# Optimization experiments

Measured on AMD Instinct MI355X. Metric: run time of the kernel, lower is better.

Reference implementation:

```python
import jax, jax.numpy as jnp
import numpy as np

# Criterion init constants
WEIGHT_START = 1e-3
WEIGHT_MAX = 5e3
START_RAMPUP = 50000
N_RAMPUP = 100000
EPS = 1e-3

B, N_CLOTH, M_OBS, N_FACES = 2, 16384, 12000, 16384


def setup_inputs() -> dict:
    key = jax.random.key(0)
    ks = jax.random.split(key, 5)
    return dict(
        cloth_curr_pos=jax.random.normal(ks[0], (B, N_CLOTH, 3), jnp.float32),
        cloth_next_pos=jax.random.normal(ks[1], (B, N_CLOTH, 3), jnp.float32),
        obstacle_curr_pos=jax.random.normal(ks[2], (B, M_OBS, 3), jnp.float32),
        obstacle_next_pos=jax.random.normal(ks[3], (B, M_OBS, 3), jnp.float32),
        obstacle_faces=jax.random.randint(ks[4], (B, N_FACES, 3), 0, M_OBS, dtype=jnp.int64),
        iter_num=60000,
    )


def _face_normals(verts, faces):
    # verts: [M,3], faces: [F,3] -> normalized face normals [F,3]
    v = verts[faces]  # [F,3(vert),3(xyz)]
    n = jnp.cross(v[:, 1] - v[:, 0], v[:, 2] - v[:, 0])
    return n / (jnp.linalg.norm(n, axis=-1, keepdims=True) + 1e-12)


def _calc_loss(curr_pos, next_pos, obs_curr, obs_next, faces):
    # face centroids at current obstacle positions: [F,3]
    face_curr = obs_curr[faces].mean(axis=-2)
    # brute-force KNN (K=1): squared euclidean distances [N,F]
    d2 = (
        jnp.sum(curr_pos * curr_pos, axis=-1, keepdims=True)
        - 2.0 * curr_pos @ face_curr.T
        + jnp.sum(face_curr * face_curr, axis=-1)[None, :]
    )
    nn_idx = jnp.argmin(d2, axis=-1)  # [N]
    # face centroids / normals at next obstacle positions
    face_next = obs_next[faces].mean(axis=-2)  # [F,3]
    fn = _face_normals(obs_next, faces)        # [F,3]
    nn_points = face_next[nn_idx]   # [N,3]
    nn_normals = fn[nn_idx]         # [N,3]
    distance = jnp.sum((next_pos - nn_points) * nn_normals, axis=-1)  # [N]
    interpenetration = jnp.maximum(EPS - distance, 0.0) ** 3
    return interpenetration.sum(), interpenetration


def reference(cloth_curr_pos, cloth_next_pos, obstacle_curr_pos, obstacle_next_pos, obstacle_faces, iter_num):
    # weight ramp (Python scalar math, matches get_weight)
    it = max(iter_num - START_RAMPUP, 0)
    progress = min(it / N_RAMPUP, 1.0)
    weight = WEIGHT_START + (WEIGHT_MAX - WEIGHT_START) * progress

    losses, per_verts = jax.vmap(_calc_loss)(
        cloth_curr_pos, cloth_next_pos, obstacle_curr_pos, obstacle_next_pos, obstacle_faces
    )
    b = cloth_curr_pos.shape[0]
    loss = losses.sum() / b * weight          # scalar
    per_vert = per_verts.sum(axis=0) / b * weight  # [N]
    return loss, per_vert
```

## Files before the change

kernel.cpp:

```cpp
#include <hip/hip_runtime.h>
#include <math.h>

#define B_ 2
#define N_ 16384
#define M_ 12000
#define F_ 16384

#define P_ 128
#define TILE_ 128
#define NCHUNK_ 8

typedef short bf16x8 __attribute__((ext_vector_type(8)));
typedef float f32x16 __attribute__((ext_vector_type(16)));

__device__ __host__ inline unsigned short bf16rn(float x) {
  unsigned int u = __float_as_uint(x);
  u = (u + 0x7FFFu + ((u >> 16) & 1u)) >> 16;
  return (unsigned short)u;
}
__device__ inline float bf16tof(unsigned short h) {
  return __uint_as_float(((unsigned int)h) << 16);
}

__device__ __forceinline__ void gload_lds16(const uint4* g, uint4* l) {
  __builtin_amdgcn_global_load_lds(
      (const __attribute__((address_space(1))) void*)g,
      (__attribute__((address_space(3))) void*)l, 16, 0, 0);
}

__global__ __launch_bounds__(128) void face_precomp(
    const float* __restrict__ obs_curr,
    const float* __restrict__ obs_next,
    const int* __restrict__ faces,
    float4* __restrict__ fcurr,
    float4* __restrict__ fnext,
    uint4* __restrict__ fpack,
    float* __restrict__ out) {
  int lane = threadIdx.x & 63;
  int half = threadIdx.x >> 6;
  int t = blockIdx.x * 64 + lane;
  if (blockIdx.x == 0 && threadIdx.x == 0) out[0] = 0.0f;
  int b = t / F_;
  const int* fidx3 = faces + 3 * (size_t)t;
  int i0 = fidx3[0];
  int i1 = fidx3[1];
  int i2 = fidx3[2];

  if (half == 0) {
    const float* oc = obs_curr + (size_t)b * M_ * 3;
    float ax = oc[3*i0], ay = oc[3*i0+1], az = oc[3*i0+2];
    float bx = oc[3*i1], by = oc[3*i1+1], bz = oc[3*i1+2];
    float cx = oc[3*i2], cy = oc[3*i2+1], cz = oc[3*i2+2];
    float gx = (ax + bx + cx) / 3.0f;
    float gy = (ay + by + cy) / 3.0f;
    float gz = (az + bz + cz) / 3.0f;
    float w = gx*gx + gy*gy + gz*gz;
    fcurr[t] = make_float4(gx, gy, gz, w);

    float fx = -2.0f * gx, fy = -2.0f * gy, fz = -2.0f * gz;
    unsigned short fhx = bf16rn(fx), flx = bf16rn(fx - bf16tof(fhx));
    unsigned short fhy = bf16rn(fy), fly = bf16rn(fy - bf16tof(fhy));
    unsigned short fhz = bf16rn(fz), flz = bf16rn(fz - bf16tof(fhz));
    unsigned short whi = bf16rn(w),  wlo = bf16rn(w - bf16tof(whi));
    uint4 r0, r1;
    r0.x = (unsigned)fhx | ((unsigned)flx << 16);
    r0.y = r0.x;
    r0.z = (unsigned)fhy | ((unsigned)fly << 16);
    r0.w = r0.z;
    r1.x = (unsigned)fhz | ((unsigned)flz << 16);
    r1.y = r1.x;
    r1.z = (unsigned)whi | ((unsigned)wlo << 16);
    r1.w = 0;
    fpack[(size_t)t * 2 + 0] = r0;
    fpack[(size_t)t * 2 + 1] = r1;
  } else {
    const float* on = obs_next + (size_t)b * M_ * 3;
    float nax = on[3*i0], nay = on[3*i0+1], naz = on[3*i0+2];
    float nbx = on[3*i1], nby = on[3*i1+1], nbz = on[3*i1+2];
    float ncx = on[3*i2], ncy = on[3*i2+1], ncz = on[3*i2+2];
    float hx = (nax + nbx + ncx) / 3.0f;
    float hy = (nay + nby + ncy) / 3.0f;
    float hz = (naz + nbz + ncz) / 3.0f;
    float e1x = nbx - nax, e1y = nby - nay, e1z = nbz - naz;
    float e2x = ncx - nax, e2y = ncy - nay, e2z = ncz - naz;
    float crx = e1y * e2z - e1z * e2y;
    float cry = e1z * e2x - e1x * e2z;
    float crz = e1x * e2y - e1y * e2x;
    float len = sqrtf(crx*crx + cry*cry + crz*crz);
    float inv = 1.0f / (len + 1e-12f);
    fnext[2 * (size_t)t + 0] = make_float4(hx, hy, hz, 0.0f);
    fnext[2 * (size_t)t + 1] = make_float4(crx*inv, cry*inv, crz*inv, 0.0f);
  }
}

__global__ __launch_bounds__(256, 4) void knn_mfma32(
    const float* __restrict__ cloth_curr,
    const uint4* __restrict__ fpack,
    float2* __restrict__ pchunk) {
  __shared__ uint4 abuf[2][256];

  int bid = blockIdx.x;
  int s   = bid & 7;
  int vb  = (bid >> 3) & 63;
  int b   = bid >> 9;
  int lane = threadIdx.x & 63;
  int wid  = threadIdx.x >> 6;
  int h = lane >> 5;
  int m = lane & 31;
  int vw = vb * 256 + wid * 64;

  const short one = (short)0x3F80;
  bf16x8 bfrag0, bfrag1;
#pragma unroll
  for (int g = 0; g < 2; ++g) {
    const float* cp = cloth_curr + ((size_t)b * N_ + vw + g * 32 + m) * 3;
    float cxx = cp[0], cyy = cp[1], czz = cp[2];
    unsigned short chx = bf16rn(cxx), clx = bf16rn(cxx - bf16tof(chx));
    unsigned short chy = bf16rn(cyy), cly = bf16rn(cyy - bf16tof(chy));
    unsigned short chz = bf16rn(czz), clz = bf16rn(czz - bf16tof(chz));
    bf16x8 tq;
    if (h == 0) {
      tq[0] = (short)chx; tq[1] = (short)chx;
      tq[2] = (short)clx; tq[3] = (short)clx;
      tq[4] = (short)chy; tq[5] = (short)chy;
      tq[6] = (short)cly; tq[7] = (short)cly;
    } else {
      tq[0] = (short)chz; tq[1] = (short)chz;
      tq[2] = (short)clz; tq[3] = (short)clz;
      tq[4] = one; tq[5] = one;
      tq[6] = 0;   tq[7] = 0;
    }
    if (g == 0) bfrag0 = tq; else bfrag1 = tq;
  }

  f32x16 zc;
#pragma unroll
  for (int k = 0; k < 16; ++k) zc[k] = 0.0f;

  const uint4* chunk = fpack + ((size_t)b * F_ + (size_t)s * 2048) * 2;

  gload_lds16(chunk + wid * 64 + lane, &abuf[0][wid * 64]);
  __syncthreads();

  float rb0 = 3.4e38f, rb1 = 3.4e38f;
  int   rp0 = 0,       rp1 = 0;

  for (int part = 0; part < 16; ++part) {
    int cur = part & 1;
    if (part < 15)
      gload_lds16(chunk + (part + 1) * 256 + wid * 64 + lane,
                  &abuf[cur ^ 1][wid * 64]);

    float r0[8], r1[8];
#pragma unroll
    for (int k = 0; k < 8; ++k) { r0[k] = 3.4e38f; r1[k] = 3.4e38f; }

    const uint4* lp = &abuf[cur][m * 2 + h];
#pragma unroll
    for (int grp = 0; grp < 2; ++grp) {
      uint4 a0 = lp[grp * 128];
      uint4 a1 = lp[grp * 128 + 64];
      bf16x8 av0 = __builtin_bit_cast(bf16x8, a0);
      bf16x8 av1 = __builtin_bit_cast(bf16x8, a1);
      f32x16 d00 = __builtin_amdgcn_mfma_f32_32x32x16_bf16(av0, bfrag0, zc, 0, 0, 0);
      f32x16 d01 = __builtin_amdgcn_mfma_f32_32x32x16_bf16(av0, bfrag1, zc, 0, 0, 0);
      f32x16 d10 = __builtin_amdgcn_mfma_f32_32x32x16_bf16(av1, bfrag0, zc, 0, 0, 0);
      f32x16 d11 = __builtin_amdgcn_mfma_f32_32x32x16_bf16(av1, bfrag1, zc, 0, 0, 0);
#pragma unroll
      for (int k = 0; k < 8; ++k) {
        r0[k] = fminf(fminf(d00[k], d00[k + 8]), r0[k]);
        r0[k] = fminf(fminf(d10[k], d10[k + 8]), r0[k]);
        r1[k] = fminf(fminf(d01[k], d01[k + 8]), r1[k]);
        r1[k] = fminf(fminf(d11[k], d11[k + 8]), r1[k]);
      }
    }
    float t0 = fminf(fminf(r0[0], r0[1]), r0[2]);
    t0 = fminf(fminf(t0, r0[3]), r0[4]);
    t0 = fminf(fminf(t0, r0[5]), r0[6]);
    float bmin0 = fminf(t0, r0[7]);
    float t1 = fminf(fminf(r1[0], r1[1]), r1[2]);
    t1 = fminf(fminf(t1, r1[3]), r1[4]);
    t1 = fminf(fminf(t1, r1[5]), r1[6]);
    float bmin1 = fminf(t1, r1[7]);
    bmin0 = fminf(bmin0, __shfl_xor(bmin0, 32, 64));
    bmin1 = fminf(bmin1, __shfl_xor(bmin1, 32, 64));

    bool u0 = bmin0 < rb0;
    rb0 = u0 ? bmin0 : rb0;
    rp0 = u0 ? part : rp0;
    bool u1 = bmin1 < rb1;
    rb1 = u1 ? bmin1 : rb1;
    rp1 = u1 ? part : rp1;

    if (part < 15) __syncthreads();
  }

  float2* pout = pchunk + ((size_t)(b * NCHUNK_ + s)) * N_ + vw;
  if (lane < 32) {
    pout[lane]      = make_float2(rb0, __int_as_float(s * 16 + rp0));
    pout[32 + lane] = make_float2(rb1, __int_as_float(s * 16 + rp1));
  }
}

__global__ __launch_bounds__(128) void epilogue(
    const float* __restrict__ cloth_curr,
    const float* __restrict__ cloth_next,
    const float4* __restrict__ fcurr,
    const float4* __restrict__ fnext,
    const float2* __restrict__ pchunk,
    const int* __restrict__ iter_num,
    float* __restrict__ out) {
  int t = blockIdx.x * 128 + threadIdx.x;
  int i = t >> 1;
  int b = t & 1;

  int it = *iter_num;
  double itc = (double)(it - 50000);
  if (itc < 0.0) itc = 0.0;
  double prog = itc / 100000.0;
  if (prog > 1.0) prog = 1.0;
  float weight = (float)(1e-3 + (5e3 - 1e-3) * prog);
  float scale = weight * 0.5f;

  const float* cp = cloth_curr + ((size_t)b * N_ + i) * 3;
  float m2x = -2.0f * cp[0];
  float m2y = -2.0f * cp[1];
  float m2z = -2.0f * cp[2];
  const float* np2 = cloth_next + ((size_t)b * N_ + i) * 3;
  float nx = np2[0], ny = np2[1], nz = np2[2];

  float best = 3.4e38f;
  int bp = 0;
#pragma unroll
  for (int c = 0; c < NCHUNK_; ++c) {
    float2 v = pchunk[((size_t)(b * NCHUNK_ + c)) * N_ + i];
    bool mm = v.x < best;
    best = mm ? v.x : best;
    bp = mm ? __float_as_int(v.y) : bp;
  }

  const float4* fpp = fcurr + (size_t)b * F_ + (size_t)bp * TILE_;
  float sbest = 3.4e38f;
  int jwin = 0;
#pragma unroll 8
  for (int j = 0; j < TILE_; ++j) {
    float4 fc = fpp[j];
    float s = fmaf(m2x, fc.x, fmaf(m2y, fc.y, fmaf(m2z, fc.z, fc.w)));
    bool u = s < sbest;
    sbest = u ? s : sbest;
    jwin = u ? j : jwin;
  }
  int fidx = bp * TILE_ + jwin;

  float4 cent = fnext[2 * ((size_t)b * F_ + fidx) + 0];
  float4 nrm  = fnext[2 * ((size_t)b * F_ + fidx) + 1];
  float dist = (nx - cent.x) * nrm.x +
               (ny - cent.y) * nrm.y +
               (nz - cent.z) * nrm.z;
  float ip = fmaxf(1e-3f - dist, 0.0f);
  float acc = ip * ip * ip * scale;

  float pair = acc + __shfl_xor(acc, 1, 64);
  if (b == 0) out[1 + i] = pair;

  float r = acc;
#pragma unroll
  for (int off = 32; off > 0; off >>= 1) r += __shfl_down(r, off, 64);
  __shared__ float wsum[2];
  int lane = threadIdx.x & 63;
  int w = threadIdx.x >> 6;
  if (lane == 0) wsum[w] = r;
  __syncthreads();
  if (threadIdx.x == 0)
    atomicAdd(out, wsum[0] + wsum[1]);
}

extern "C" void kernel_launch(void* const* d_in, const int* in_sizes, int n_in,
                              void* d_out, int out_size, void* d_ws, size_t ws_size,
                              hipStream_t stream) {
  const float* cloth_curr = (const float*)d_in[0];
  const float* cloth_next = (const float*)d_in[1];
  const float* obs_curr   = (const float*)d_in[2];
  const float* obs_next   = (const float*)d_in[3];
  const int*   faces      = (const int*)d_in[4];
  const int*   iter_num   = (const int*)d_in[5];
  float* out = (float*)d_out;

  char* w = (char*)d_ws;
  float4* fcurr = (float4*)(w);
  float4* fnext = (float4*)(w + 524288);
  uint4*  fpack = (uint4*)(w + 1572864);
  float2* pchunk = (float2*)(w + 3670016);

  face_precomp<<<(B_ * F_) / 64, 128, 0, stream>>>(
      obs_curr, obs_next, faces, fcurr, fnext, fpack, out);

  knn_mfma32<<<1024, 256, 0, stream>>>(cloth_curr, fpack, pchunk);

  epilogue<<<(2 * N_ + 127) / 128, 128, 0, stream>>>(
      cloth_curr, cloth_next, fcurr, fnext, pchunk, iter_num, out);
}
```

Before: 104.5 us.

## Fuse epilogue into KNN kernel via last-block-done atomic counter

Removes the separate epilogue launch. Each KNN block bumps a per-vertex-block counter, and the last of the 16 blocks (8 chunks times 2 batches) for a 256-vertex group does the chunk reduction, the tile rescan, the interpenetration and the sum. The counter is reset inside face_precomp. This saves one kernel launch and its gap, at the cost of threadfences, atomics and a serial tail done by the last-arriving blocks.

```diff
diff --git a/kernel.cpp b/kernel.cpp
--- a/kernel.cpp
+++ b/kernel.cpp
@@ -35,11 +35,13 @@
     float4* __restrict__ fcurr,
     float4* __restrict__ fnext,
     uint4* __restrict__ fpack,
-    float* __restrict__ out) {
+    float* __restrict__ out,
+    int* __restrict__ cnt) {
   int lane = threadIdx.x & 63;
   int half = threadIdx.x >> 6;
   int t = blockIdx.x * 64 + lane;
   if (blockIdx.x == 0 && threadIdx.x == 0) out[0] = 0.0f;
+  if (blockIdx.x == 0 && half == 1) cnt[lane] = 0;
   int b = t / F_;
   const int* fidx3 = faces + 3 * (size_t)t;
   int i0 = fidx3[0];
@@ -96,7 +98,13 @@
 __global__ __launch_bounds__(256, 4) void knn_mfma32(
     const float* __restrict__ cloth_curr,
     const uint4* __restrict__ fpack,
-    float2* __restrict__ pchunk) {
+    float2* __restrict__ pchunk,
+    const float* __restrict__ cloth_next,
+    const float4* __restrict__ fcurr,
+    const float4* __restrict__ fnext,
+    const int* __restrict__ iter_num,
+    float* __restrict__ out,
+    int* __restrict__ cnt) {
   __shared__ uint4 abuf[2][256];
 
   int bid = blockIdx.x;
@@ -200,79 +208,95 @@
     pout[lane]      = make_float2(rb0, __int_as_float(s * 16 + rp0));
     pout[32 + lane] = make_float2(rb1, __int_as_float(s * 16 + rp1));
   }
-}
-
-__global__ __launch_bounds__(128) void epilogue(
-    const float* __restrict__ cloth_curr,
-    const float* __restrict__ cloth_next,
-    const float4* __restrict__ fcurr,
-    const float4* __restrict__ fnext,
-    const float2* __restrict__ pchunk,
-    const int* __restrict__ iter_num,
-    float* __restrict__ out) {
-  int t = blockIdx.x * 128 + threadIdx.x;
-  int i = t >> 1;
-  int b = t & 1;
-
-  int it = *iter_num;
-  double itc = (double)(it - 50000);
+
+  __syncthreads();
+  __shared__ int lastflag;
+  if (threadIdx.x == 0) {
+    __threadfence();
+    int old = atomicAdd(&cnt[vb], 1);
+    lastflag = (old == 15);
+  }
+  __syncthreads();
+  if (!lastflag) return;
+  __threadfence();
+
+  int tid = threadIdx.x;
+  int i = vb * 256 + tid;
+
+  int itv = *iter_num;
+  double itc = (double)(itv - 50000);
   if (itc < 0.0) itc = 0.0;
   double prog = itc / 100000.0;
   if (prog > 1.0) prog = 1.0;
   float weight = (float)(1e-3 + (5e3 - 1e-3) * prog);
   float scale = weight * 0.5f;
 
-  const float* cp = cloth_curr + ((size_t)b * N_ + i) * 3;
-  float m2x = -2.0f * cp[0];
-  float m2y = -2.0f * cp[1];
-  float m2z = -2.0f * cp[2];
-  const float* np2 = cloth_next + ((size_t)b * N_ + i) * 3;
-  float nx = np2[0], ny = np2[1], nz = np2[2];
-
-  float best = 3.4e38f;
-  int bp = 0;
+  float best0 = 3.4e38f, best1 = 3.4e38f;
+  int bp0 = 0, bp1 = 0;
 #pragma unroll
   for (int c = 0; c < NCHUNK_; ++c) {
-    float2 v = pchunk[((size_t)(b * NCHUNK_ + c)) * N_ + i];
-    bool mm = v.x < best;
-    best = mm ? v.x : best;
-    bp = mm ? __float_as_int(v.y) : bp;
-  }
-
-  const float4* fpp = fcurr + (size_t)b * F_ + (size_t)bp * TILE_;
-  float sbest = 3.4e38f;
-  int jwin = 0;
-#pragma unroll 8
+    float2 v0 = pchunk[((size_t)c) * N_ + i];
+    float2 v1 = pchunk[((size_t)(NCHUNK_ + c)) * N_ + i];
+    bool m0 = v0.x < best0;
+    best0 = m0 ? v0.x : best0;
+    bp0 = m0 ? __float_as_int(v0.y) : bp0;
+    bool m1 = v1.x < best1;
+    best1 = m1 ? v1.x : best1;
+    bp1 = m1 ? __float_as_int(v1.y) : bp1;
+  }
+
+  const float* cp0 = cloth_curr + (size_t)i * 3;
+  const float* cp1 = cloth_curr + ((size_t)N_ + i) * 3;
+  float ax0 = -2.0f * cp0[0], ay0 = -2.0f * cp0[1], az0 = -2.0f * cp0[2];
+  float ax1 = -2.0f * cp1[0], ay1 = -2.0f * cp1[1], az1 = -2.0f * cp1[2];
+  const float* nq0 = cloth_next + (size_t)i * 3;
+  const float* nq1 = cloth_next + ((size_t)N_ + i) * 3;
+  float nx0 = nq0[0], ny0 = nq0[1], nz0 = nq0[2];
+  float nx1 = nq1[0], ny1 = nq1[1], nz1 = nq1[2];
+
+  const float4* fA = fcurr + (size_t)bp0 * TILE_;
+  const float4* fB = fcurr + (size_t)F_ + (size_t)bp1 * TILE_;
+  float s0 = 3.4e38f, s1 = 3.4e38f;
+  int j0 = 0, j1 = 0;
+#pragma unroll 4
   for (int j = 0; j < TILE_; ++j) {
-    float4 fc = fpp[j];
-    float s = fmaf(m2x, fc.x, fmaf(m2y, fc.y, fmaf(m2z, fc.z, fc.w)));
-    bool u = s < sbest;
-    sbest = u ? s : sbest;
-    jwin = u ? j : jwin;
-  }
-  int fidx = bp * TILE_ + jwin;
-
-  float4 cent = fnext[2 * ((size_t)b * F_ + fidx) + 0];
-  float4 nrm  = fnext[2 * ((size_t)b * F_ + fidx) + 1];
-  float dist = (nx - cent.x) * nrm.x +
-               (ny - cent.y) * nrm.y +
-               (nz - cent.z) * nrm.z;
-  float ip = fmaxf(1e-3f - dist, 0.0f);
-  float acc = ip * ip * ip * scale;
-
-  float pair = acc + __shfl_xor(acc, 1, 64);
-  if (b == 0) out[1 + i] = pair;
-
-  float r = acc;
+    float4 fa = fA[j];
+    float fb_s;
+    float4 fb = fB[j];
+    float sa = fmaf(ax0, fa.x, fmaf(ay0, fa.y, fmaf(az0, fa.z, fa.w)));
+    fb_s = fmaf(ax1, fb.x, fmaf(ay1, fb.y, fmaf(az1, fb.z, fb.w)));
+    bool u0 = sa < s0;
+    s0 = u0 ? sa : s0;
+    j0 = u0 ? j : j0;
+    bool u1 = fb_s < s1;
+    s1 = u1 ? fb_s : s1;
+    j1 = u1 ? j : j1;
+  }
+  int f0 = bp0 * TILE_ + j0;
+  int f1 = F_ + bp1 * TILE_ + j1;
+
+  float4 c0 = fnext[2 * (size_t)f0 + 0];
+  float4 nr0 = fnext[2 * (size_t)f0 + 1];
+  float4 c1 = fnext[2 * (size_t)f1 + 0];
+  float4 nr1 = fnext[2 * (size_t)f1 + 1];
+  float d0 = (nx0 - c0.x) * nr0.x + (ny0 - c0.y) * nr0.y + (nz0 - c0.z) * nr0.z;
+  float d1 = (nx1 - c1.x) * nr1.x + (ny1 - c1.y) * nr1.y + (nz1 - c1.z) * nr1.z;
+  float ip0 = fmaxf(1e-3f - d0, 0.0f);
+  float ip1 = fmaxf(1e-3f - d1, 0.0f);
+  float acc0 = ip0 * ip0 * ip0 * scale;
+  float acc1 = ip1 * ip1 * ip1 * scale;
+  float pair = acc0 + acc1;
+
+  out[1 + i] = pair;
+
+  float r = pair;
 #pragma unroll
   for (int off = 32; off > 0; off >>= 1) r += __shfl_down(r, off, 64);
-  __shared__ float wsum[2];
-  int lane = threadIdx.x & 63;
-  int w = threadIdx.x >> 6;
-  if (lane == 0) wsum[w] = r;
+  __shared__ float wsum[4];
+  if (lane == 0) wsum[wid] = r;
   __syncthreads();
   if (threadIdx.x == 0)
-    atomicAdd(out, wsum[0] + wsum[1]);
+    atomicAdd(out, (wsum[0] + wsum[1]) + (wsum[2] + wsum[3]));
 }
 
 extern "C" void kernel_launch(void* const* d_in, const int* in_sizes, int n_in,
@@ -291,12 +315,11 @@
   float4* fnext = (float4*)(w + 524288);
   uint4*  fpack = (uint4*)(w + 1572864);
   float2* pchunk = (float2*)(w + 3670016);
+  int*    cnt   = (int*)(w + 5767168);
 
   face_precomp<<<(B_ * F_) / 64, 128, 0, stream>>>(
-      obs_curr, obs_next, faces, fcurr, fnext, fpack, out);
-
-  knn_mfma32<<<1024, 256, 0, stream>>>(cloth_curr, fpack, pchunk);
-
-  epilogue<<<(2 * N_ + 127) / 128, 128, 0, stream>>>(
-      cloth_curr, cloth_next, fcurr, fnext, pchunk, iter_num, out);
-}
+      obs_curr, obs_next, faces, fcurr, fnext, fpack, out, cnt);
+
+  knn_mfma32<<<1024, 256, 0, stream>>>(
+      cloth_curr, fpack, pchunk, cloth_next, fcurr, fnext, iter_num, out, cnt);
+}
```

Result: slower. 185.9 us (+78.0%).
